# Kernel optimization log

Measured on AMD Instinct MI355X. Metric: run time of the kernel, lower is better.

The kernel has to match this reference:

```python
import jax, jax.numpy as jnp
import numpy as np

I, H, O = 64, 256, 24
B, S = 256, 1024


def setup_inputs() -> dict:
    key = jax.random.key(0)
    ks = jax.random.split(key, 9)
    s = lambda *d: 1.0 / np.sqrt(d[0])
    return {
        "x": jax.random.normal(ks[0], (B, S, I), dtype=jnp.float32),
        "Wi": jax.random.normal(ks[1], (I, 4 * H), dtype=jnp.float32) * s(I),
        "Wh": jax.random.normal(ks[2], (H, 4 * H), dtype=jnp.float32) * s(H),
        "b": jnp.zeros((4 * H,), dtype=jnp.float32),
        "attn_W": jax.random.normal(ks[3], (H, H), dtype=jnp.float32) * s(H),
        "attn_b": jnp.zeros((H,), dtype=jnp.float32),
        "v": jax.random.uniform(ks[4], (H,), dtype=jnp.float32) * 0.01,
        "fc_W": jax.random.normal(ks[5], (H, O), dtype=jnp.float32) * s(H),
        "fc_b": jnp.zeros((O,), dtype=jnp.float32),
    }


def _lstm(x, Wi, Wh, b):
    # x: [B, S, I] -> outputs [B, S, H]
    xW = jnp.einsum("bsi,ij->bsj", x, Wi)  # precompute input projections
    Bsz = x.shape[0]
    h0 = jnp.zeros((Bsz, H), x.dtype)
    c0 = jnp.zeros((Bsz, H), x.dtype)

    def step(carry, xt):
        c, h = carry
        z = xt + h @ Wh + b  # [B, 4H]
        i, f, g, o = jnp.split(z, 4, axis=-1)
        c = jax.nn.sigmoid(f) * c + jax.nn.sigmoid(i) * jnp.tanh(g)
        h = jax.nn.sigmoid(o) * jnp.tanh(c)
        return (c, h), h

    _, hs = jax.lax.scan(step, (c0, h0), jnp.swapaxes(xW, 0, 1))
    return jnp.swapaxes(hs, 0, 1)  # [B, S, H]


def reference(x, Wi, Wh, b, attn_W, attn_b, v, fc_W, fc_b):
    lstm_out = _lstm(x, Wi, Wh, b)  # [B, S, H]
    energy = jnp.tanh(lstm_out @ attn_W + attn_b)  # [B, S, H]
    scores = jnp.einsum("bsh,h->bs", energy, v)
    attn = jax.nn.softmax(scores, axis=1)  # [B, S]
    context = jnp.einsum("bs,bsh->bh", attn, lstm_out)
    return context @ fc_W + fc_b  # [B, O]
```

## Files before the change

### kernel.cpp

```cpp
#include <hip/hip_runtime.h>

#define BB 256
#define SS 1024
#define II 64
#define HH 256
#define OO 24
#define NG 16
#define NP 16
#define BT 16

typedef __attribute__((ext_vector_type(8))) short short8;
typedef __attribute__((ext_vector_type(4))) float f32x4;
typedef unsigned long long ull;

#define H_CAP  8192
#define SP_CAP 16384

#define A_HI 0
#define A_LO 8192
#define Z_OF 16384
#define E_OF 20480
#define SMEM_BYTES 98304

#define MFMA(a,b,c) __builtin_amdgcn_mfma_f32_16x16x32_bf16(a,b,c,0,0,0)

__device__ __forceinline__ float fsig(float x)  { return 1.f/(1.f+__expf(-x)); }
__device__ __forceinline__ float ftanh(float x) { return 1.f - 2.f/(__expf(2.f*x)+1.f); }

__device__ __forceinline__ unsigned rne_bf16(float x){
    unsigned u = __float_as_uint(x);
    return (u + 0x7FFFu + ((u>>16)&1u)) >> 16;
}
__device__ __forceinline__ void split_bf(float x, unsigned &hi, unsigned &lo){
    hi = rne_bf16(x);
    lo = rne_bf16(x - __uint_as_float(hi<<16));
}

union U4 { unsigned u[4]; short8 s; };

__device__ __forceinline__ void pack8(const float* v, short8 &H, short8 &L){
    U4 h_, l_;
    #pragma unroll
    for (int i = 0; i < 4; ++i) {
        unsigned a,b,c,d;
        split_bf(v[2*i], a, b); split_bf(v[2*i+1], c, d);
        h_.u[i] = a | (c<<16);
        l_.u[i] = b | (d<<16);
    }
    H = h_.s; L = l_.s;
}

__device__ __forceinline__ ull cld(const ull* p){
    return __hip_atomic_load(p, __ATOMIC_RELAXED, __HIP_MEMORY_SCOPE_AGENT);
}
__device__ __forceinline__ void cst(ull* p, ull v){
    __hip_atomic_store(p, v, __ATOMIC_RELAXED, __HIP_MEMORY_SCOPE_AGENT);
}

__global__ __launch_bounds__(256, 1)
void lstm_fused_kernel(const float* __restrict__ x,  const float* __restrict__ Wi,
                       const float* __restrict__ Wh, const float* __restrict__ bias,
                       const float* __restrict__ aW, const float* __restrict__ ab,
                       const float* __restrict__ av,
                       ull* __restrict__ hx, ull* __restrict__ spx,
                       float* __restrict__ ctxg)
{
    __shared__ __align__(16) char smem[SMEM_BYTES];
    __shared__ int sdead;

    const int tid = threadIdx.x;
    const int w = tid >> 6;
    const int l = tid & 63;
    const int p = blockIdx.x >> 4;
    const int g = blockIdx.x & 15;
    const int b0 = g * BT;

    if (tid == 0) sdead = 0;
    __syncthreads();

    const int n = l & 15;
    const int gcol = w*256 + p*16 + n;
    const int gb = (l>>4)*4 + w;
    const int gd = n;

    short8 BwhH[8], BwhL[8];
    #pragma unroll
    for (int ks = 0; ks < 8; ++ks) {
        U4 H, L;
        #pragma unroll
        for (int i2 = 0; i2 < 4; ++i2) {
            int k0 = ks*32 + (l>>4)*8 + i2*2;
            unsigned h0,l0,h1,l1;
            split_bf(Wh[(size_t)k0*1024 + gcol], h0, l0);
            split_bf(Wh[(size_t)(k0+1)*1024 + gcol], h1, l1);
            H.u[i2] = h0 | (h1<<16);
            L.u[i2] = l0 | (l1<<16);
        }
        BwhH[ks] = H.s; BwhL[ks] = L.s;
    }
    short8 BwiH[2], BwiL[2];
    #pragma unroll
    for (int ks = 0; ks < 2; ++ks) {
        U4 H, L;
        #pragma unroll
        for (int i2 = 0; i2 < 4; ++i2) {
            int k0 = ks*32 + (l>>4)*8 + i2*2;
            unsigned h0,l0,h1,l1;
            split_bf(Wi[(size_t)k0*1024 + gcol], h0, l0);
            split_bf(Wi[(size_t)(k0+1)*1024 + gcol], h1, l1);
            H.u[i2] = h0 | (h1<<16);
            L.u[i2] = l0 | (l1<<16);
        }
        BwiH[ks] = H.s; BwiL[ks] = L.s;
    }
    short8 BwaH[2], BwaL[2];
    #pragma unroll
    for (int j = 0; j < 2; ++j) {
        int ks = 2*w + j;
        U4 H, L;
        #pragma unroll
        for (int i2 = 0; i2 < 4; ++i2) {
            int k0 = ks*32 + (l>>4)*8 + i2*2;
            unsigned h0,l0,h1,l1;
            split_bf(aW[(size_t)k0*256 + p*16 + n], h0, l0);
            split_bf(aW[(size_t)(k0+1)*256 + p*16 + n], h1, l1);
            H.u[i2] = h0 | (h1<<16);
            L.u[i2] = l0 | (l1<<16);
        }
        BwaH[j] = H.s; BwaL[j] = L.s;
    }
    const float bb  = bias[gcol];
    const float vj  = av[p*16 + gd];
    const float abj = ab[p*16 + gd];

    const int po    = tid >> 3;
    const int pbase = (tid & 7) * 2;
    const int wa0 = (po>>2)*1024 + ((po&3)*16 + pbase)*16;
    const int wa1 = wa0 + 16;

    const int D = p*16 + gd;
    const int tau   = (gb>>1) | ((D>>3)<<3);
    const int j_pub = ((gb&1)<<3) | (D&7);

    const int xb = l & 15;
    const int xoct = l >> 4;

    float c_state = 0.f, h1v = 0.f, h2v = 0.f;
    float m_run = -1.0e30f, l_run = 0.f, ctx = 0.f;

    float* zl = (float*)(smem + Z_OF);
    float* el = (float*)(smem + E_OF);

    for (int t = 0; t < SS; ++t) {
        const int par = t & 1;
        const float* xrow = x + ((size_t)(b0 + xb) * SS + t) * II + xoct*8;
        float xv0[8], xv1[8];
        *(float4*)&xv0[0] = *(const float4*)(xrow);
        *(float4*)&xv0[4] = *(const float4*)(xrow + 4);
        *(float4*)&xv1[0] = *(const float4*)(xrow + 32);
        *(float4*)&xv1[4] = *(const float4*)(xrow + 36);

        ull hv[16]; ull spr = 0;
        const ull* hr = hx + ((size_t)(((t-1)&1)*NG + g) * 16) * 256 + tid;
        if (t > 0) {
            #pragma unroll
            for (int j = 0; j < 16; ++j) hv[j] = cld(hr + j*256);
        }
        ull* spp = spx + (size_t)par*4096 + g*256 + gb*16 + gd;
        if (t > 1) spr = cld(spp);

        short8 XH0, XL0, XH1, XL1;
        pack8(xv0, XH0, XL0);
        pack8(xv1, XH1, XL1);
        f32x4 zacc = {bb,bb,bb,bb};
        zacc = MFMA(XH0, BwiH[0], zacc);
        zacc = MFMA(XH0, BwiL[0], zacc);
        zacc = MFMA(XL0, BwiH[0], zacc);
        zacc = MFMA(XH1, BwiH[1], zacc);
        zacc = MFMA(XH1, BwiL[1], zacc);
        zacc = MFMA(XL1, BwiH[1], zacc);

        if (t > 0) {
            const unsigned texp = (unsigned)t;
            unsigned need = 0xFFFFu;
            int rounds = 0;
            while (true) {
                unsigned nn = 0;
                #pragma unroll
                for (int e = 0; e < 16; ++e)
                    if (need & (1u<<e))
                        if ((unsigned)(hv[e]>>32) != texp) nn |= (1u<<e);
                need = nn;
                if (!need || sdead) break;
                if (++rounds > H_CAP) { sdead = 1; break; }
                #pragma unroll
                for (int e = 0; e < 16; ++e)
                    if (need & (1u<<e)) hv[e] = cld(hr + e*256);
            }
            float va[16];
            #pragma unroll
            for (int e = 0; e < 16; ++e) va[e] = __uint_as_float((unsigned)hv[e]);
            short8 H0,L0,H1,L1;
            pack8(&va[0], H0, L0);
            pack8(&va[8], H1, L1);
            *(short8*)(smem + A_HI + wa0) = H0;
            *(short8*)(smem + A_LO + wa0) = L0;
            *(short8*)(smem + A_HI + wa1) = H1;
            *(short8*)(smem + A_LO + wa1) = L1;
        }
        __syncthreads();

        f32x4 zacc1 = {0.f,0.f,0.f,0.f};
        f32x4 eacc  = {0.f,0.f,0.f,0.f};
        if (t > 0) {
            #pragma unroll
            for (int ks = 0; ks < 8; ++ks) {
                short8 ah = *(const short8*)(smem + A_HI + ks*1024 + l*16);
                short8 al = *(const short8*)(smem + A_LO + ks*1024 + l*16);
                if ((ks & 1) == 0) {
                    zacc = MFMA(ah, BwhH[ks], zacc);
                    zacc = MFMA(ah, BwhL[ks], zacc);
                    zacc = MFMA(al, BwhH[ks], zacc);
                } else {
                    zacc1 = MFMA(ah, BwhH[ks], zacc1);
                    zacc1 = MFMA(ah, BwhL[ks], zacc1);
                    zacc1 = MFMA(al, BwhH[ks], zacc1);
                }
                if ((ks>>1) == w) {
                    int jj = ks & 1;
                    eacc = MFMA(ah, BwaH[jj], eacc);
                    eacc = MFMA(ah, BwaL[jj], eacc);
                    eacc = MFMA(al, BwaH[jj], eacc);
                }
            }
        }
        #pragma unroll
        for (int r = 0; r < 4; ++r) zl[w*256 + r*64 + l] = zacc[r] + zacc1[r];
        if (t > 0) {
            #pragma unroll
            for (int r = 0; r < 4; ++r) el[w*256 + r*64 + l] = eacc[r];
        }
        __syncthreads();

        float z0 = zl[0*256 + w*64 + l];
        float z1 = zl[1*256 + w*64 + l];
        float z2 = zl[2*256 + w*64 + l];
        float z3 = zl[3*256 + w*64 + l];
        float ig = fsig(z0), fg = fsig(z1), gv = ftanh(z2), og = fsig(z3);
        c_state = fg*c_state + ig*gv;
        float h = og * ftanh(c_state);

        cst(hx + ((size_t)(par*NG + g) * 16 + j_pub) * 256 + tau,
            ((ull)(unsigned)(t+1) << 32) | (ull)__float_as_uint(h));

        if (t > 0) {
            float e = el[0*256+w*64+l] + el[1*256+w*64+l]
                    + el[2*256+w*64+l] + el[3*256+w*64+l] + abj;
            float scp = vj * ftanh(e);
            scp += __shfl_xor(scp,1); scp += __shfl_xor(scp,2);
            scp += __shfl_xor(scp,4); scp += __shfl_xor(scp,8);
            if (gd == 0)
                cst(spx + (size_t)((t-1)&1)*4096 + g*256 + gb*16 + p,
                    ((ull)(unsigned)t << 32) | (ull)__float_as_uint(scp));
        }
        if (t > 1) {
            const unsigned texp = (unsigned)(t-1);
            int it = 0;
            while ((unsigned)(spr>>32) != texp) {
                if (sdead || ++it > SP_CAP) { sdead = 1; break; }
                spr = cld(spp);
            }
            float s = __uint_as_float((unsigned)spr);
            s += __shfl_xor(s,1); s += __shfl_xor(s,2);
            s += __shfl_xor(s,4); s += __shfl_xor(s,8);
            float m_new = fmaxf(m_run, s);
            float sc = __expf(m_run - m_new);
            float wt = __expf(s - m_new);
            l_run = l_run*sc + wt;
            ctx   = ctx*sc + wt*h2v;
            m_run = m_new;
        }
        h2v = h1v; h1v = h;
    }

    {
        const ull* hr = hx + ((size_t)(((SS-1)&1)*NG + g) * 16) * 256 + tid;
        ull hv[16];
        #pragma unroll
        for (int j = 0; j < 16; ++j) hv[j] = cld(hr + j*256);
        const unsigned texp = (unsigned)SS;
        unsigned need = 0xFFFFu;
        int rounds = 0;
        while (true) {
            unsigned nn = 0;
            #pragma unroll
            for (int e = 0; e < 16; ++e)
                if (need & (1u<<e))
                    if ((unsigned)(hv[e]>>32) != texp) nn |= (1u<<e);
            need = nn;
            if (!need || sdead) break;
            if (++rounds > H_CAP) { sdead = 1; break; }
            #pragma unroll
            for (int e = 0; e < 16; ++e)
                if (need & (1u<<e)) hv[e] = cld(hr + e*256);
        }
        float va[16];
        #pragma unroll
        for (int e = 0; e < 16; ++e) va[e] = __uint_as_float((unsigned)hv[e]);
        short8 H0,L0,H1,L1;
        pack8(&va[0], H0, L0);
        pack8(&va[8], H1, L1);
        *(short8*)(smem + A_HI + wa0) = H0;
        *(short8*)(smem + A_LO + wa0) = L0;
        *(short8*)(smem + A_HI + wa1) = H1;
        *(short8*)(smem + A_LO + wa1) = L1;
        __syncthreads();

        f32x4 eacc = {0.f,0.f,0.f,0.f};
        #pragma unroll
        for (int ks = 0; ks < 8; ++ks) {
            if ((ks>>1) == w) {
                short8 ah = *(const short8*)(smem + A_HI + ks*1024 + l*16);
                short8 al = *(const short8*)(smem + A_LO + ks*1024 + l*16);
                int jj = ks & 1;
                eacc = MFMA(ah, BwaH[jj], eacc);
                eacc = MFMA(ah, BwaL[jj], eacc);
                eacc = MFMA(al, BwaH[jj], eacc);
            }
        }
        #pragma unroll
        for (int r = 0; r < 4; ++r) el[w*256 + r*64 + l] = eacc[r];
        __syncthreads();

        {
            ull* spp2 = spx + (size_t)(SS&1)*4096 + g*256 + gb*16 + gd;
            ull spr = cld(spp2);
            const unsigned te2 = (unsigned)(SS-1);
            int it = 0;
            while ((unsigned)(spr>>32) != te2) {
                if (sdead || ++it > SP_CAP) { sdead = 1; break; }
                spr = cld(spp2);
            }
            float s = __uint_as_float((unsigned)spr);
            s += __shfl_xor(s,1); s += __shfl_xor(s,2);
            s += __shfl_xor(s,4); s += __shfl_xor(s,8);
            float m_new = fmaxf(m_run, s);
            float sc = __expf(m_run - m_new);
            float wt = __expf(s - m_new);
            l_run = l_run*sc + wt;
            ctx   = ctx*sc + wt*h2v;
            m_run = m_new;
        }
        h2v = h1v;
        float e = el[0*256+w*64+l] + el[1*256+w*64+l]
                + el[2*256+w*64+l] + el[3*256+w*64+l] + abj;
        float scp = vj * ftanh(e);
        scp += __shfl_xor(scp,1); scp += __shfl_xor(scp,2);
        scp += __shfl_xor(scp,4); scp += __shfl_xor(scp,8);
        if (gd == 0)
            cst(spx + (size_t)((SS-1)&1)*4096 + g*256 + gb*16 + p,
                ((ull)(unsigned)SS << 32) | (ull)__float_as_uint(scp));
    }

    {
        ull* spp2 = spx + (size_t)((SS-1)&1)*4096 + g*256 + gb*16 + gd;
        ull spr = cld(spp2);
        const unsigned texp = (unsigned)SS;
        int it = 0;
        while ((unsigned)(spr>>32) != texp) {
            if (sdead || ++it > SP_CAP) { sdead = 1; break; }
            spr = cld(spp2);
        }
        float s = __uint_as_float((unsigned)spr);
        s += __shfl_xor(s,1); s += __shfl_xor(s,2);
        s += __shfl_xor(s,4); s += __shfl_xor(s,8);
        float m_new = fmaxf(m_run, s);
        float sc = __expf(m_run - m_new);
        float wt = __expf(s - m_new);
        l_run = l_run*sc + wt;
        ctx   = ctx*sc + wt*h2v;

        ctxg[(size_t)(b0+gb)*HH + p*16 + gd] = ctx / l_run;
    }
}

__global__ __launch_bounds__(64)
void finalize_kernel(const float* __restrict__ ctxg, const float* __restrict__ fcW,
                     const float* __restrict__ fcb, float* __restrict__ out)
{
    __shared__ float cs[HH];
    const int b = blockIdx.x, tid = threadIdx.x;
    *(float4*)&cs[tid*4] = *(const float4*)&ctxg[(size_t)b*HH + tid*4];
    __syncthreads();
    if (tid < OO) {
        float a = fcb[tid];
        #pragma unroll 8
        for (int d = 0; d < HH; ++d) a = fmaf(cs[d], fcW[d*OO + tid], a);
        out[b*OO + tid] = a;
    }
}

extern "C" void kernel_launch(void* const* d_in, const int* in_sizes, int n_in,
                              void* d_out, int out_size, void* d_ws, size_t ws_size,
                              hipStream_t stream)
{
    const float* x      = (const float*)d_in[0];
    const float* Wi     = (const float*)d_in[1];
    const float* Wh     = (const float*)d_in[2];
    const float* bias   = (const float*)d_in[3];
    const float* attn_W = (const float*)d_in[4];
    const float* attn_b = (const float*)d_in[5];
    const float* v      = (const float*)d_in[6];
    const float* fc_W   = (const float*)d_in[7];
    const float* fc_b   = (const float*)d_in[8];
    float* out = (float*)d_out;

    ull*   hx   = (ull*)d_ws;
    ull*   spx  = hx + 2*NG*16*256;
    float* ctxg = (float*)(spx + 8192);

    hipMemsetAsync(hx, 0, (2*NG*16*256 + 8192) * sizeof(ull), stream);

    lstm_fused_kernel<<<dim3(NG*NP), dim3(256), 0, stream>>>(
        x, Wi, Wh, bias, attn_W, attn_b, v, hx, spx, ctxg);
    finalize_kernel<<<dim3(BB), dim3(64), 0, stream>>>(ctxg, fc_W, fc_b, out);
}
```

Baseline: 3.523 ms.

## Repartition LSTM to 8 batch rows by 32 hidden units per block

Changes the work split from 16 batch groups by 16 hidden slices to 32 batch groups by 8 slices. Each block now holds twice as many Wh/Wi/attn weight columns in registers and runs two MFMA column tiles per step. Each cross-block h exchange now polls 8 peers instead of 16, which shortens the per-step global synchronisation wait. Publishers also pre-split h into bf16 hi/lo before storing, which removes the unpack work on the consumer side. The cost is doubled per-block MFMA work and register pressure, and half of each MFMA's 16 batch rows now carry padding.

```diff
diff --git a/kernel.cpp b/kernel.cpp
--- a/kernel.cpp
+++ b/kernel.cpp
@@ -5,9 +5,9 @@
 #define II 64
 #define HH 256
 #define OO 24
-#define NG 16
-#define NP 16
-#define BT 16
+#define NG 32
+#define NP 8
+#define BT 8
 
 typedef __attribute__((ext_vector_type(8))) short short8;
 typedef __attribute__((ext_vector_type(4))) float f32x4;
@@ -19,7 +19,7 @@
 #define A_HI 0
 #define A_LO 8192
 #define Z_OF 16384
-#define E_OF 20480
+#define E_OF 24576
 #define SMEM_BYTES 98304
 
 #define MFMA(a,b,c) __builtin_amdgcn_mfma_f32_16x16x32_bf16(a,b,c,0,0,0)
@@ -71,78 +71,88 @@
     const int tid = threadIdx.x;
     const int w = tid >> 6;
     const int l = tid & 63;
-    const int p = blockIdx.x >> 4;
-    const int g = blockIdx.x & 15;
+    const int p = blockIdx.x & 7;
+    const int g = blockIdx.x >> 3;
     const int b0 = g * BT;
 
     if (tid == 0) sdead = 0;
     __syncthreads();
 
     const int n = l & 15;
-    const int gcol = w*256 + p*16 + n;
-    const int gb = (l>>4)*4 + w;
-    const int gd = n;
-
-    short8 BwhH[8], BwhL[8];
+
+    const int sb  = tid >> 5;
+    const int sjd = tid & 31;
+
+    short8 BwhH[16], BwhL[16];
     #pragma unroll
-    for (int ks = 0; ks < 8; ++ks) {
-        U4 H, L;
-        #pragma unroll
-        for (int i2 = 0; i2 < 4; ++i2) {
-            int k0 = ks*32 + (l>>4)*8 + i2*2;
-            unsigned h0,l0,h1,l1;
-            split_bf(Wh[(size_t)k0*1024 + gcol], h0, l0);
-            split_bf(Wh[(size_t)(k0+1)*1024 + gcol], h1, l1);
-            H.u[i2] = h0 | (h1<<16);
-            L.u[i2] = l0 | (l1<<16);
-        }
-        BwhH[ks] = H.s; BwhL[ks] = L.s;
-    }
-    short8 BwiH[2], BwiL[2];
+    for (int ti = 0; ti < 2; ++ti) {
+        const int gc = w*256 + p*32 + ti*16 + n;
+        #pragma unroll
+        for (int ks = 0; ks < 8; ++ks) {
+            U4 H, L;
+            #pragma unroll
+            for (int i2 = 0; i2 < 4; ++i2) {
+                int k0 = ks*32 + (l>>4)*8 + i2*2;
+                unsigned h0,l0,h1,l1;
+                split_bf(Wh[(size_t)k0*1024 + gc], h0, l0);
+                split_bf(Wh[(size_t)(k0+1)*1024 + gc], h1, l1);
+                H.u[i2] = h0 | (h1<<16);
+                L.u[i2] = l0 | (l1<<16);
+            }
+            BwhH[ti*8+ks] = H.s; BwhL[ti*8+ks] = L.s;
+        }
+    }
+    short8 BwiH[4], BwiL[4];
     #pragma unroll
-    for (int ks = 0; ks < 2; ++ks) {
-        U4 H, L;
-        #pragma unroll
-        for (int i2 = 0; i2 < 4; ++i2) {
-            int k0 = ks*32 + (l>>4)*8 + i2*2;
-            unsigned h0,l0,h1,l1;
-            split_bf(Wi[(size_t)k0*1024 + gcol], h0, l0);
-            split_bf(Wi[(size_t)(k0+1)*1024 + gcol], h1, l1);
-            H.u[i2] = h0 | (h1<<16);
-            L.u[i2] = l0 | (l1<<16);
-        }
-        BwiH[ks] = H.s; BwiL[ks] = L.s;
-    }
-    short8 BwaH[2], BwaL[2];
+    for (int ti = 0; ti < 2; ++ti) {
+        const int gc = w*256 + p*32 + ti*16 + n;
+        #pragma unroll
+        for (int ks = 0; ks < 2; ++ks) {
+            U4 H, L;
+            #pragma unroll
+            for (int i2 = 0; i2 < 4; ++i2) {
+                int k0 = ks*32 + (l>>4)*8 + i2*2;
+                unsigned h0,l0,h1,l1;
+                split_bf(Wi[(size_t)k0*1024 + gc], h0, l0);
+                split_bf(Wi[(size_t)(k0+1)*1024 + gc], h1, l1);
+                H.u[i2] = h0 | (h1<<16);
+                L.u[i2] = l0 | (l1<<16);
+            }
+            BwiH[ti*2+ks] = H.s; BwiL[ti*2+ks] = L.s;
+        }
+    }
+    short8 BwaH[4], BwaL[4];
     #pragma unroll
-    for (int j = 0; j < 2; ++j) {
-        int ks = 2*w + j;
-        U4 H, L;
-        #pragma unroll
-        for (int i2 = 0; i2 < 4; ++i2) {
-            int k0 = ks*32 + (l>>4)*8 + i2*2;
-            unsigned h0,l0,h1,l1;
-            split_bf(aW[(size_t)k0*256 + p*16 + n], h0, l0);
-            split_bf(aW[(size_t)(k0+1)*256 + p*16 + n], h1, l1);
-            H.u[i2] = h0 | (h1<<16);
-            L.u[i2] = l0 | (l1<<16);
-        }
-        BwaH[j] = H.s; BwaL[j] = L.s;
-    }
-    const float bb  = bias[gcol];
-    const float vj  = av[p*16 + gd];
-    const float abj = ab[p*16 + gd];
-
-    const int po    = tid >> 3;
-    const int pbase = (tid & 7) * 2;
-    const int wa0 = (po>>2)*1024 + ((po&3)*16 + pbase)*16;
-    const int wa1 = wa0 + 16;
-
-    const int D = p*16 + gd;
-    const int tau   = (gb>>1) | ((D>>3)<<3);
-    const int j_pub = ((gb&1)<<3) | (D&7);
-
-    const int xb = l & 15;
+    for (int ti = 0; ti < 2; ++ti) {
+        #pragma unroll
+        for (int j = 0; j < 2; ++j) {
+            int ks = 2*w + j;
+            U4 H, L;
+            #pragma unroll
+            for (int i2 = 0; i2 < 4; ++i2) {
+                int k0 = ks*32 + (l>>4)*8 + i2*2;
+                unsigned h0,l0,h1,l1;
+                split_bf(aW[(size_t)k0*256 + p*32 + ti*16 + n], h0, l0);
+                split_bf(aW[(size_t)(k0+1)*256 + p*32 + ti*16 + n], h1, l1);
+                H.u[i2] = h0 | (h1<<16);
+                L.u[i2] = l0 | (l1<<16);
+            }
+            BwaH[ti*2+j] = H.s; BwaL[ti*2+j] = L.s;
+        }
+    }
+    const float bb0 = bias[w*256 + p*32 + n];
+    const float bb1 = bias[w*256 + p*32 + 16 + n];
+    const float vj  = av[p*32 + sjd];
+    const float abj = ab[p*32 + sjd];
+
+    const int po_c = tid & 31, bb_c = tid >> 5;
+    const int wa = ((po_c>>2)*64 + (po_c&3)*16 + bb_c)*16;
+
+    const int D = p*32 + sjd;
+    const int j_pub = D & 7;
+    const int tau   = sb*32 + (D>>3);
+
+    const int xb = l & 7;
     const int xoct = l >> 4;
 
     float c_state = 0.f, h1v = 0.f, h2v = 0.f;
@@ -150,6 +160,7 @@
 
     float* zl = (float*)(smem + Z_OF);
     float* el = (float*)(smem + E_OF);
+    const int zi = (sjd>>4)*256 + (sb&3)*64 + (sb>>2)*16 + (sjd&15);
 
     for (int t = 0; t < SS; ++t) {
         const int par = t & 1;
@@ -160,107 +171,110 @@
         *(float4*)&xv1[0] = *(const float4*)(xrow + 32);
         *(float4*)&xv1[4] = *(const float4*)(xrow + 36);
 
-        ull hv[16]; ull spr = 0;
-        const ull* hr = hx + ((size_t)(((t-1)&1)*NG + g) * 16) * 256 + tid;
+        ull hv[8]; ull spr = 0;
+        const ull* hr = hx + ((size_t)(((t-1)&1)*NG + g) * 8) * 256 + tid;
         if (t > 0) {
             #pragma unroll
-            for (int j = 0; j < 16; ++j) hv[j] = cld(hr + j*256);
-        }
-        ull* spp = spx + (size_t)par*4096 + g*256 + gb*16 + gd;
+            for (int j = 0; j < 8; ++j) hv[j] = cld(hr + j*256);
+        }
+        ull* spp = spx + (size_t)par*2048 + g*64 + sb*8 + (sjd&7);
         if (t > 1) spr = cld(spp);
 
         short8 XH0, XL0, XH1, XL1;
         pack8(xv0, XH0, XL0);
         pack8(xv1, XH1, XL1);
-        f32x4 zacc = {bb,bb,bb,bb};
-        zacc = MFMA(XH0, BwiH[0], zacc);
-        zacc = MFMA(XH0, BwiL[0], zacc);
-        zacc = MFMA(XL0, BwiH[0], zacc);
-        zacc = MFMA(XH1, BwiH[1], zacc);
-        zacc = MFMA(XH1, BwiL[1], zacc);
-        zacc = MFMA(XL1, BwiH[1], zacc);
+        f32x4 zA0 = {bb0,bb0,bb0,bb0}, zA1 = {0.f,0.f,0.f,0.f};
+        f32x4 zB0 = {bb1,bb1,bb1,bb1}, zB1 = {0.f,0.f,0.f,0.f};
+        zA0 = MFMA(XH0, BwiH[0], zA0); zA0 = MFMA(XH0, BwiL[0], zA0); zA0 = MFMA(XL0, BwiH[0], zA0);
+        zA0 = MFMA(XH1, BwiH[1], zA0); zA0 = MFMA(XH1, BwiL[1], zA0); zA0 = MFMA(XL1, BwiH[1], zA0);
+        zB0 = MFMA(XH0, BwiH[2], zB0); zB0 = MFMA(XH0, BwiL[2], zB0); zB0 = MFMA(XL0, BwiH[2], zB0);
+        zB0 = MFMA(XH1, BwiH[3], zB0); zB0 = MFMA(XH1, BwiL[3], zB0); zB0 = MFMA(XL1, BwiH[3], zB0);
 
         if (t > 0) {
             const unsigned texp = (unsigned)t;
-            unsigned need = 0xFFFFu;
+            unsigned need = 0xFFu;
             int rounds = 0;
             while (true) {
                 unsigned nn = 0;
                 #pragma unroll
-                for (int e = 0; e < 16; ++e)
+                for (int e = 0; e < 8; ++e)
                     if (need & (1u<<e))
                         if ((unsigned)(hv[e]>>32) != texp) nn |= (1u<<e);
                 need = nn;
                 if (!need || sdead) break;
                 if (++rounds > H_CAP) { sdead = 1; break; }
                 #pragma unroll
-                for (int e = 0; e < 16; ++e)
+                for (int e = 0; e < 8; ++e)
                     if (need & (1u<<e)) hv[e] = cld(hr + e*256);
             }
-            float va[16];
-            #pragma unroll
-            for (int e = 0; e < 16; ++e) va[e] = __uint_as_float((unsigned)hv[e]);
-            short8 H0,L0,H1,L1;
-            pack8(&va[0], H0, L0);
-            pack8(&va[8], H1, L1);
-            *(short8*)(smem + A_HI + wa0) = H0;
-            *(short8*)(smem + A_LO + wa0) = L0;
-            *(short8*)(smem + A_HI + wa1) = H1;
-            *(short8*)(smem + A_LO + wa1) = L1;
+            U4 H, L;
+            #pragma unroll
+            for (int i = 0; i < 4; ++i) {
+                unsigned a = (unsigned)hv[2*i], b_ = (unsigned)hv[2*i+1];
+                H.u[i] = (a>>16) | (b_ & 0xFFFF0000u);
+                L.u[i] = (a & 0xFFFFu) | (b_<<16);
+            }
+            *(short8*)(smem + A_HI + wa) = H.s;
+            *(short8*)(smem + A_LO + wa) = L.s;
         }
         __syncthreads();
 
-        f32x4 zacc1 = {0.f,0.f,0.f,0.f};
-        f32x4 eacc  = {0.f,0.f,0.f,0.f};
+        f32x4 eA = {0.f,0.f,0.f,0.f}, eB = {0.f,0.f,0.f,0.f};
         if (t > 0) {
             #pragma unroll
             for (int ks = 0; ks < 8; ++ks) {
                 short8 ah = *(const short8*)(smem + A_HI + ks*1024 + l*16);
                 short8 al = *(const short8*)(smem + A_LO + ks*1024 + l*16);
                 if ((ks & 1) == 0) {
-                    zacc = MFMA(ah, BwhH[ks], zacc);
-                    zacc = MFMA(ah, BwhL[ks], zacc);
-                    zacc = MFMA(al, BwhH[ks], zacc);
+                    zA0 = MFMA(ah, BwhH[ks], zA0);   zA0 = MFMA(ah, BwhL[ks], zA0);   zA0 = MFMA(al, BwhH[ks], zA0);
+                    zB0 = MFMA(ah, BwhH[8+ks], zB0); zB0 = MFMA(ah, BwhL[8+ks], zB0); zB0 = MFMA(al, BwhH[8+ks], zB0);
                 } else {
-                    zacc1 = MFMA(ah, BwhH[ks], zacc1);
-                    zacc1 = MFMA(ah, BwhL[ks], zacc1);
-                    zacc1 = MFMA(al, BwhH[ks], zacc1);
+                    zA1 = MFMA(ah, BwhH[ks], zA1);   zA1 = MFMA(ah, BwhL[ks], zA1);   zA1 = MFMA(al, BwhH[ks], zA1);
+                    zB1 = MFMA(ah, BwhH[8+ks], zB1); zB1 = MFMA(ah, BwhL[8+ks], zB1); zB1 = MFMA(al, BwhH[8+ks], zB1);
                 }
                 if ((ks>>1) == w) {
                     int jj = ks & 1;
-                    eacc = MFMA(ah, BwaH[jj], eacc);
-                    eacc = MFMA(ah, BwaL[jj], eacc);
-                    eacc = MFMA(al, BwaH[jj], eacc);
+                    eA = MFMA(ah, BwaH[jj], eA);   eA = MFMA(ah, BwaL[jj], eA);   eA = MFMA(al, BwaH[jj], eA);
+                    eB = MFMA(ah, BwaH[2+jj], eB); eB = MFMA(ah, BwaL[2+jj], eB); eB = MFMA(al, BwaH[2+jj], eB);
                 }
             }
         }
         #pragma unroll
-        for (int r = 0; r < 4; ++r) zl[w*256 + r*64 + l] = zacc[r] + zacc1[r];
+        for (int r = 0; r < 4; ++r) {
+            zl[w*512 +       r*64 + l] = zA0[r] + zA1[r];
+            zl[w*512 + 256 + r*64 + l] = zB0[r] + zB1[r];
+        }
         if (t > 0) {
             #pragma unroll
-            for (int r = 0; r < 4; ++r) el[w*256 + r*64 + l] = eacc[r];
+            for (int r = 0; r < 4; ++r) {
+                el[w*512 +       r*64 + l] = eA[r];
+                el[w*512 + 256 + r*64 + l] = eB[r];
+            }
         }
         __syncthreads();
 
-        float z0 = zl[0*256 + w*64 + l];
-        float z1 = zl[1*256 + w*64 + l];
-        float z2 = zl[2*256 + w*64 + l];
-        float z3 = zl[3*256 + w*64 + l];
+        float z0 = zl[0*512 + zi];
+        float z1 = zl[1*512 + zi];
+        float z2 = zl[2*512 + zi];
+        float z3 = zl[3*512 + zi];
         float ig = fsig(z0), fg = fsig(z1), gv = ftanh(z2), og = fsig(z3);
         c_state = fg*c_state + ig*gv;
         float h = og * ftanh(c_state);
 
-        cst(hx + ((size_t)(par*NG + g) * 16 + j_pub) * 256 + tau,
-            ((ull)(unsigned)(t+1) << 32) | (ull)__float_as_uint(h));
+        {
+            unsigned hhi, hlo; split_bf(h, hhi, hlo);
+            cst(hx + ((size_t)(par*NG + g) * 8 + j_pub) * 256 + tau,
+                ((ull)(unsigned)(t+1) << 32) | (ull)((hhi<<16)|hlo));
+        }
 
         if (t > 0) {
-            float e = el[0*256+w*64+l] + el[1*256+w*64+l]
-                    + el[2*256+w*64+l] + el[3*256+w*64+l] + abj;
+            float e = el[0*512+zi] + el[1*512+zi] + el[2*512+zi] + el[3*512+zi] + abj;
             float scp = vj * ftanh(e);
             scp += __shfl_xor(scp,1); scp += __shfl_xor(scp,2);
             scp += __shfl_xor(scp,4); scp += __shfl_xor(scp,8);
-            if (gd == 0)
-                cst(spx + (size_t)((t-1)&1)*4096 + g*256 + gb*16 + p,
+            scp += __shfl_xor(scp,16);
+            if (sjd == 0)
+                cst(spx + (size_t)((t-1)&1)*2048 + g*64 + sb*8 + p,
                     ((ull)(unsigned)t << 32) | (ull)__float_as_uint(scp));
         }
         if (t > 1) {
@@ -271,8 +285,7 @@
                 spr = cld(spp);
             }
             float s = __uint_as_float((unsigned)spr);
-            s += __shfl_xor(s,1); s += __shfl_xor(s,2);
-            s += __shfl_xor(s,4); s += __shfl_xor(s,8);
+            s += __shfl_xor(s,1); s += __shfl_xor(s,2); s += __shfl_xor(s,4);
             float m_new = fmaxf(m_run, s);
             float sc = __expf(m_run - m_new);
             float wt = __expf(s - m_new);
@@ -284,56 +297,57 @@
     }
 
     {
-        const ull* hr = hx + ((size_t)(((SS-1)&1)*NG + g) * 16) * 256 + tid;
-        ull hv[16];
-        #pragma unroll
-        for (int j = 0; j < 16; ++j) hv[j] = cld(hr + j*256);
+        const ull* hr = hx + ((size_t)(((SS-1)&1)*NG + g) * 8) * 256 + tid;
+        ull hv[8];
+        #pragma unroll
+        for (int j = 0; j < 8; ++j) hv[j] = cld(hr + j*256);
         const unsigned texp = (unsigned)SS;
-        unsigned need = 0xFFFFu;
+        unsigned need = 0xFFu;
         int rounds = 0;
         while (true) {
             unsigned nn = 0;
             #pragma unroll
-            for (int e = 0; e < 16; ++e)
+            for (int e = 0; e < 8; ++e)
                 if (need & (1u<<e))
                     if ((unsigned)(hv[e]>>32) != texp) nn |= (1u<<e);
             need = nn;
             if (!need || sdead) break;
             if (++rounds > H_CAP) { sdead = 1; break; }
             #pragma unroll
-            for (int e = 0; e < 16; ++e)
+            for (int e = 0; e < 8; ++e)
                 if (need & (1u<<e)) hv[e] = cld(hr + e*256);
         }
-        float va[16];
-        #pragma unroll
-        for (int e = 0; e < 16; ++e) va[e] = __uint_as_float((unsigned)hv[e]);
-        short8 H0,L0,H1,L1;
-        pack8(&va[0], H0, L0);
-        pack8(&va[8], H1, L1);
-        *(short8*)(smem + A_HI + wa0) = H0;
-        *(short8*)(smem + A_LO + wa0) = L0;
-        *(short8*)(smem + A_HI + wa1) = H1;
-        *(short8*)(smem + A_LO + wa1) = L1;
+        U4 H, L;
+        #pragma unroll
+        for (int i = 0; i < 4; ++i) {
+            unsigned a = (unsigned)hv[2*i], b_ = (unsigned)hv[2*i+1];
+            H.u[i] = (a>>16) | (b_ & 0xFFFF0000u);
+            L.u[i] = (a & 0xFFFFu) | (b_<<16);
+        }
+        *(short8*)(smem + A_HI + wa) = H.s;
+        *(short8*)(smem + A_LO + wa) = L.s;
         __syncthreads();
 
-        f32x4 eacc = {0.f,0.f,0.f,0.f};
+        f32x4 eA = {0.f,0.f,0.f,0.f}, eB = {0.f,0.f,0.f,0.f};
         #pragma unroll
         for (int ks = 0; ks < 8; ++ks) {
             if ((ks>>1) == w) {
                 short8 ah = *(const short8*)(smem + A_HI + ks*1024 + l*16);
                 short8 al = *(const short8*)(smem + A_LO + ks*1024 + l*16);
                 int jj = ks & 1;
-                eacc = MFMA(ah, BwaH[jj], eacc);
-                eacc = MFMA(ah, BwaL[jj], eacc);
-                eacc = MFMA(al, BwaH[jj], eacc);
-            }
-        }
-        #pragma unroll
-        for (int r = 0; r < 4; ++r) el[w*256 + r*64 + l] = eacc[r];
+                eA = MFMA(ah, BwaH[jj], eA);   eA = MFMA(ah, BwaL[jj], eA);   eA = MFMA(al, BwaH[jj], eA);
+                eB = MFMA(ah, BwaH[2+jj], eB); eB = MFMA(ah, BwaL[2+jj], eB); eB = MFMA(al, BwaH[2+jj], eB);
+            }
+        }
+        #pragma unroll
+        for (int r = 0; r < 4; ++r) {
+            el[w*512 +       r*64 + l] = eA[r];
+            el[w*512 + 256 + r*64 + l] = eB[r];
+        }
         __syncthreads();
 
         {
-            ull* spp2 = spx + (size_t)(SS&1)*4096 + g*256 + gb*16 + gd;
+            ull* spp2 = spx + (size_t)(SS&1)*2048 + g*64 + sb*8 + (sjd&7);
             ull spr = cld(spp2);
             const unsigned te2 = (unsigned)(SS-1);
             int it = 0;
@@ -342,8 +356,7 @@
                 spr = cld(spp2);
             }
             float s = __uint_as_float((unsigned)spr);
-            s += __shfl_xor(s,1); s += __shfl_xor(s,2);
-            s += __shfl_xor(s,4); s += __shfl_xor(s,8);
+            s += __shfl_xor(s,1); s += __shfl_xor(s,2); s += __shfl_xor(s,4);
             float m_new = fmaxf(m_run, s);
             float sc = __expf(m_run - m_new);
             float wt = __expf(s - m_new);
@@ -352,18 +365,18 @@
             m_run = m_new;
         }
         h2v = h1v;
-        float e = el[0*256+w*64+l] + el[1*256+w*64+l]
-                + el[2*256+w*64+l] + el[3*256+w*64+l] + abj;
+        float e = el[0*512+zi] + el[1*512+zi] + el[2*512+zi] + el[3*512+zi] + abj;
         float scp = vj * ftanh(e);
         scp += __shfl_xor(scp,1); scp += __shfl_xor(scp,2);
         scp += __shfl_xor(scp,4); scp += __shfl_xor(scp,8);
-        if (gd == 0)
-            cst(spx + (size_t)((SS-1)&1)*4096 + g*256 + gb*16 + p,
+        scp += __shfl_xor(scp,16);
+        if (sjd == 0)
+            cst(spx + (size_t)((SS-1)&1)*2048 + g*64 + sb*8 + p,
                 ((ull)(unsigned)SS << 32) | (ull)__float_as_uint(scp));
     }
 
     {
-        ull* spp2 = spx + (size_t)((SS-1)&1)*4096 + g*256 + gb*16 + gd;
+        ull* spp2 = spx + (size_t)((SS-1)&1)*2048 + g*64 + sb*8 + (sjd&7);
         ull spr = cld(spp2);
         const unsigned texp = (unsigned)SS;
         int it = 0;
@@ -372,15 +385,14 @@
             spr = cld(spp2);
         }
         float s = __uint_as_float((unsigned)spr);
-        s += __shfl_xor(s,1); s += __shfl_xor(s,2);
-        s += __shfl_xor(s,4); s += __shfl_xor(s,8);
+        s += __shfl_xor(s,1); s += __shfl_xor(s,2); s += __shfl_xor(s,4);
         float m_new = fmaxf(m_run, s);
         float sc = __expf(m_run - m_new);
         float wt = __expf(s - m_new);
         l_run = l_run*sc + wt;
         ctx   = ctx*sc + wt*h2v;
 
-        ctxg[(size_t)(b0+gb)*HH + p*16 + gd] = ctx / l_run;
+        ctxg[(size_t)(b0+sb)*HH + p*32 + sjd] = ctx / l_run;
     }
 }
 
@@ -416,10 +428,10 @@
     float* out = (float*)d_out;
 
     ull*   hx   = (ull*)d_ws;
-    ull*   spx  = hx + 2*NG*16*256;
-    float* ctxg = (float*)(spx + 8192);
-
-    hipMemsetAsync(hx, 0, (2*NG*16*256 + 8192) * sizeof(ull), stream);
+    ull*   spx  = hx + 2*NG*8*256;
+    float* ctxg = (float*)(spx + 4096);
+
+    hipMemsetAsync(hx, 0, (2*NG*8*256 + 4096) * sizeof(ull), stream);
 
     lstm_fused_kernel<<<dim3(NG*NP), dim3(256), 0, stream>>>(
         x, Wi, Wh, bias, attn_W, attn_b, v, hx, spx, ctxg);
```

After: 3.473 ms. No clear change (-1.4%).
